# Kernel tuning notes

Measured on AMD Instinct MI355X. Metric: run time of the kernel, lower is better.

Reference implementation:

```python
import jax, jax.numpy as jnp
import numpy as np

N_AGENTS = 16      # args['num_agents']
BATCH = 8192       # args['n_rollout_threads'] -> number of independent graphs
OBS = 64           # cent_obs_shape[0] // n_nodes
HID = 128          # args['hidden_sizes'][0]
N_LAYERS = 2       # args['n_layers']
USE_RES = True     # args['use_res']


def _build_edges():
    # complete graph (no self loops) per graph, block-diagonal over BATCH graphs
    i, j = np.meshgrid(np.arange(N_AGENTS), np.arange(N_AGENTS), indexing='ij')
    m = i != j
    bs, bd = i[m], j[m]                      # [240]
    off = (np.arange(BATCH) * N_AGENTS)[:, None]
    src = (bs[None, :] + off).ravel().astype(np.int32)  # [BATCH*240]
    dst = (bd[None, :] + off).ravel().astype(np.int32)
    return src, dst


def setup_inputs() -> dict:
    key = jax.random.key(0)
    ks = jax.random.split(key, 5)
    N = BATCH * N_AGENTS
    src, dst = _build_edges()
    return {
        'cent_obs': jax.random.normal(ks[0], (N, OBS), jnp.float32),
        'w_emb': jax.random.normal(ks[1], (OBS, HID), jnp.float32) / np.sqrt(OBS).astype(np.float32),
        'b_emb': jnp.zeros((HID,), jnp.float32),
        'w_gcn': jax.random.normal(ks[2], (N_LAYERS, HID, HID), jnp.float32) / np.sqrt(HID).astype(np.float32),
        'b_gcn': jnp.zeros((N_LAYERS, HID), jnp.float32),
        'w_fc1': jax.random.normal(ks[3], (HID, 1), jnp.float32) / np.sqrt(HID).astype(np.float32),
        'b_fc1': jnp.zeros((1,), jnp.float32),
        'edge_src': jnp.asarray(src),
        'edge_dst': jnp.asarray(dst),
    }


def reference(cent_obs, w_emb, b_emb, w_gcn, b_gcn, w_fc1, b_fc1, edge_src, edge_dst):
    N = cent_obs.shape[0]
    # embedding_in
    x = cent_obs @ w_emb + b_emb                           # [N, HID]
    # GCNConv normalization with added self-loops (PyG default, sym norm)
    loop = jnp.arange(N, dtype=edge_src.dtype)
    src = jnp.concatenate([edge_src, loop])
    dst = jnp.concatenate([edge_dst, loop])
    deg = jax.ops.segment_sum(jnp.ones_like(dst, dtype=x.dtype), dst, num_segments=N)
    inv_sqrt = jax.lax.rsqrt(deg)
    norm = (inv_sqrt[src] * inv_sqrt[dst])[:, None]        # [E+N, 1]
    for l in range(N_LAYERS):
        h = x @ w_gcn[l]                                   # linear transform
        agg = jax.ops.segment_sum(h[src] * norm, dst, num_segments=N) + b_gcn[l]
        x = jnp.tanh(agg + x if USE_RES else agg)
    value = x @ w_fc1 + b_fc1                              # [N, 1]
    value = value.reshape(BATCH, -1)                       # [BATCH, n_nodes]
    return value.mean(axis=1).reshape(-1, 1)               # [BATCH, 1]
```

## Files before the change

kernel.cpp:

```cpp
#include <hip/hip_runtime.h>


#define N_GRAPHS 8192
#define BLOCK    512
#define GPB      16
#define NBLOCKS  (N_GRAPHS / GPB)

typedef __attribute__((ext_vector_type(8)))  short short8;
typedef __attribute__((ext_vector_type(4)))  float floatx4;
typedef __attribute__((ext_vector_type(16))) float floatx16;

#define MFMA16(a, b, c) __builtin_amdgcn_mfma_f32_16x16x32_bf16((a), (b), (c), 0, 0, 0)
#define MFMA32(a, b, c) __builtin_amdgcn_mfma_f32_32x32x16_bf16((a), (b), (c), 0, 0, 0)

#define EMB_LO   1024
#define GCN_BASE 2048
#define GCN_LO   2048

union fragu { unsigned int u[4]; short8 s8; };

__device__ __forceinline__ unsigned fbits(float x) {
  union { float f; unsigned u; } v; v.f = x; return v.u;
}
__device__ __forceinline__ float bitsf(unsigned u) {
  union { float f; unsigned u; } v; v.u = u; return v.f;
}
__device__ __forceinline__ void bsplit(float x, short& hi, short& lo) {
  unsigned hb = fbits(x) & 0xFFFF0000u;
  hi = (short)(hb >> 16);
  lo = (short)(fbits(x - bitsf(hb)) >> 16);
}
__device__ __forceinline__ unsigned hpack(unsigned b_odd, unsigned b_even) {
  return __builtin_amdgcn_perm(b_odd, b_even, 0x07060302u);
}
__device__ __forceinline__ void mk_frags(float4 a, float4 b, short8& hi, short8& lo) {
  fragu H, L;
  H.u[0] = hpack(fbits(a.y), fbits(a.x));
  H.u[1] = hpack(fbits(a.w), fbits(a.z));
  H.u[2] = hpack(fbits(b.y), fbits(b.x));
  H.u[3] = hpack(fbits(b.w), fbits(b.z));
  float l0 = a.x - bitsf(fbits(a.x) & 0xFFFF0000u);
  float l1 = a.y - bitsf(fbits(a.y) & 0xFFFF0000u);
  float l2 = a.z - bitsf(fbits(a.z) & 0xFFFF0000u);
  float l3 = a.w - bitsf(fbits(a.w) & 0xFFFF0000u);
  float l4 = b.x - bitsf(fbits(b.x) & 0xFFFF0000u);
  float l5 = b.y - bitsf(fbits(b.y) & 0xFFFF0000u);
  float l6 = b.z - bitsf(fbits(b.z) & 0xFFFF0000u);
  float l7 = b.w - bitsf(fbits(b.w) & 0xFFFF0000u);
  L.u[0] = hpack(fbits(l1), fbits(l0));
  L.u[1] = hpack(fbits(l3), fbits(l2));
  L.u[2] = hpack(fbits(l5), fbits(l4));
  L.u[3] = hpack(fbits(l7), fbits(l6));
  hi = H.s8; lo = L.s8;
}
__device__ __forceinline__ float fast_tanh(float z) {
  float e = __expf(2.0f * z);
  return 1.0f - __fdividef(2.0f, e + 1.0f);
}

__global__ __launch_bounds__(256) void gcn_prep(
    const float* __restrict__ w_emb, const float* __restrict__ w_gcn,
    unsigned short* __restrict__ wsS)
{
  int idx = blockIdx.x * 256 + threadIdx.x;
  if (idx >= 40960) return;
  int f = idx >> 3, j = idx & 7;
  const float* src;
  int hi_f, lo_f;
  if (f < 1024) {
    int ks = f >> 8, t = (f >> 6) & 3, L = f & 63;
    int k0 = ks * 16 + (L >> 5) * 8;
    int n  = t * 32 + (L & 31);
    src = w_emb + k0 * 128 + n;
    hi_f = f; lo_f = f + EMB_LO;
  } else {
    int f2 = f - 1024;
    int l = f2 >> 11, r = f2 & 2047;
    int kc = r >> 9, nt = (r >> 6) & 7, L = r & 63;
    int k0 = kc * 32 + (L >> 4) * 8;
    int n  = nt * 16 + (L & 15);
    src = w_gcn + l * 16384 + k0 * 128 + n;
    hi_f = GCN_BASE + l * 4096 + r; lo_f = hi_f + GCN_LO;
  }
  short h, l_;
  bsplit(src[j * 128], h, l_);
  wsS[hi_f * 8 + j] = (unsigned short)h;
  wsS[lo_f * 8 + j] = (unsigned short)l_;
}

__global__ __launch_bounds__(BLOCK, 4) void gcn_main(
    const float* __restrict__ obs,
    const float* __restrict__ b_emb,
    const float* __restrict__ b_gcn,
    const float* __restrict__ w_fc1,
    const float* __restrict__ b_fc1,
    const short8* __restrict__ tab,
    float* __restrict__ out)
{
  __shared__ short8 sEmb[2048];
  __shared__ short  sA[2 * 4 * 16 * 40];
  __shared__ float  sH[16][132];

  const int tid = threadIdx.x;
  const int w   = tid >> 6;
  const int L   = tid & 63;
  const int m32 = L & 31;
  const int kh  = L >> 5;
  const int c16 = L & 15;
  const int q   = L >> 4;
  const int gw  = blockIdx.x * GPB + 2 * w;

  const float* op = obs + (gw * 16 + m32) * 64 + kh * 8;
  float4 oa0 = *(const float4*)(op);
  float4 oa1 = *(const float4*)(op + 4);
  float4 ob0 = *(const float4*)(op + 16);
  float4 ob1 = *(const float4*)(op + 20);

  #pragma unroll
  for (int i = 0; i < 4; ++i) sEmb[i * BLOCK + tid] = tab[i * BLOCK + tid];

  floatx16 x[4];
  #pragma unroll
  for (int t = 0; t < 4; ++t) {
    float b = b_emb[t * 32 + m32];
    #pragma unroll
    for (int r = 0; r < 16; ++r) x[t][r] = b;
  }
  __syncthreads();

  #pragma unroll
  for (int s = 0; s < 4; ++s) {
    short8 ah, al;
    mk_frags(oa0, oa1, ah, al);
    oa0 = ob0; oa1 = ob1;
    if (s < 2) {
      ob0 = *(const float4*)(op + (s + 2) * 16);
      ob1 = *(const float4*)(op + (s + 2) * 16 + 4);
    }
    #pragma unroll
    for (int t = 0; t < 4; ++t) {
      int idx = (s * 4 + t) * 64 + L;
      short8 bh = sEmb[idx];
      short8 bl = sEmb[idx + EMB_LO];
      x[t] = MFMA32(ah, bh, x[t]);
      x[t] = MFMA32(al, bh, x[t]);
      x[t] = MFMA32(ah, bl, x[t]);
    }
  }

  #pragma unroll 1
  for (int l = 0; l < 2; ++l) {
    const short8* tbase = tab + GCN_BASE + l * 4096 + w * 64 + L;
    short8 bh[4], bl[4];
    #pragma unroll
    for (int kc = 0; kc < 4; ++kc) {
      bh[kc] = tbase[kc * 512];
      bl[kc] = tbase[kc * 512 + GCN_LO];
    }

    #pragma unroll
    for (int t = 0; t < 4; ++t) {
      float s0 = x[t][0], s1 = x[t][8];
      #pragma unroll
      for (int r = 1; r < 8; ++r) { s0 += x[t][r]; s1 += x[t][r + 8]; }
      s0 += __shfl_xor(s0, 32);
      s1 += __shfl_xor(s1, 32);
      s0 *= 0.0625f; s1 *= 0.0625f;
      #pragma unroll
      for (int rr = 0; rr < 2; ++rr) {
        float v = rr ? s1 : s0;
        unsigned hb = fbits(v) & 0xFFFF0000u;
        unsigned vb = (kh == 0) ? hb : fbits(v - bitsf(hb));
        unsigned nb = (unsigned)__shfl_xor((int)vb, 1);
        unsigned pw = hpack(nb, vb);
        if ((m32 & 1) == 0) {
          int si = kh * 2560 + t * 640 + (2 * w + rr) * 40 + m32;
          *(unsigned int*)&sA[si] = pw;
        }
      }
    }
    __syncthreads();

    floatx4 h = {0.f, 0.f, 0.f, 0.f};
    #pragma unroll
    for (int kc = 0; kc < 4; ++kc) {
      short8 ah = *(const short8*)&sA[kc * 640 + c16 * 40 + q * 8];
      short8 al = *(const short8*)&sA[2560 + kc * 640 + c16 * 40 + q * 8];
      h = MFMA16(ah, bh[kc], h);
      h = MFMA16(al, bh[kc], h);
      h = MFMA16(ah, bl[kc], h);
    }
    #pragma unroll
    for (int r = 0; r < 4; ++r)
      sH[q * 4 + r][w * 16 + c16] = h[r];
    __syncthreads();

    #pragma unroll
    for (int t = 0; t < 4; ++t) {
      float b  = b_gcn[l * 128 + t * 32 + m32];
      float zA = sH[2 * w][t * 32 + m32] + b;
      float zB = sH[2 * w + 1][t * 32 + m32] + b;
      #pragma unroll
      for (int r = 0; r < 8; ++r) {
        x[t][r]     = fast_tanh(x[t][r] + zA);
        x[t][r + 8] = fast_tanh(x[t][r + 8] + zB);
      }
    }
  }

  float vA = 0.f, vB = 0.f;
  #pragma unroll
  for (int t = 0; t < 4; ++t) {
    float wf = w_fc1[t * 32 + m32];
    float sA_ = 0.f, sB_ = 0.f;
    #pragma unroll
    for (int r = 0; r < 8; ++r) { sA_ += x[t][r]; sB_ += x[t][r + 8]; }
    vA = fmaf(sA_, wf, vA);
    vB = fmaf(sB_, wf, vB);
  }
  #pragma unroll
  for (int d = 32; d >= 1; d >>= 1) {
    vA += __shfl_xor(vA, d);
    vB += __shfl_xor(vB, d);
  }
  if (L == 0) {
    float bf = b_fc1[0];
    out[gw]     = vA * 0.0625f + bf;
    out[gw + 1] = vB * 0.0625f + bf;
  }
}

extern "C" void kernel_launch(void* const* d_in, const int* in_sizes, int n_in,
                              void* d_out, int out_size, void* d_ws, size_t ws_size,
                              hipStream_t stream) {
  const float* obs    = (const float*)d_in[0];
  const float* w_emb  = (const float*)d_in[1];
  const float* b_emb  = (const float*)d_in[2];
  const float* w_gcn  = (const float*)d_in[3];
  const float* b_gcn  = (const float*)d_in[4];
  const float* w_fc1  = (const float*)d_in[5];
  const float* b_fc1  = (const float*)d_in[6];
  float* out = (float*)d_out;

  gcn_prep<<<160, 256, 0, stream>>>(w_emb, w_gcn, (unsigned short*)d_ws);
  gcn_main<<<NBLOCKS, BLOCK, 0, stream>>>(obs, b_emb, b_gcn, w_fc1, b_fc1,
                                          (const short8*)d_ws, out);
}
```

Measured before the change: 120.3 us.

## Switch embedding to 16x16 MFMA with one graph per wave, raise occupancy

The embedding GEMM moves from 32x32x16 MFMA to 16x16x32 MFMA. Each wave now owns one graph instead of two, which shrinks per-thread accumulator state from four floatx16 to eight floatx4. The launch bounds raise the target to 6 blocks per CU, with twice as many blocks of half the graphs, and the GCN weight fragments are double-buffered instead of all preloaded. The goal is better latency hiding through higher occupancy and lower register pressure. The cost is extra shared-memory zero-padding and sync overhead per graph, and the prep kernel becomes thread-per-fragment.

```diff
diff --git a/kernel.cpp b/kernel.cpp
--- a/kernel.cpp
+++ b/kernel.cpp
@@ -3,15 +3,13 @@
 
 #define N_GRAPHS 8192
 #define BLOCK    512
-#define GPB      16
+#define GPB      8
 #define NBLOCKS  (N_GRAPHS / GPB)
 
-typedef __attribute__((ext_vector_type(8)))  short short8;
-typedef __attribute__((ext_vector_type(4)))  float floatx4;
-typedef __attribute__((ext_vector_type(16))) float floatx16;
+typedef __attribute__((ext_vector_type(8))) short short8;
+typedef __attribute__((ext_vector_type(4))) float floatx4;
 
 #define MFMA16(a, b, c) __builtin_amdgcn_mfma_f32_16x16x32_bf16((a), (b), (c), 0, 0, 0)
-#define MFMA32(a, b, c) __builtin_amdgcn_mfma_f32_32x32x16_bf16((a), (b), (c), 0, 0, 0)
 
 #define EMB_LO   1024
 #define GCN_BASE 2048
@@ -62,33 +60,33 @@
     const float* __restrict__ w_emb, const float* __restrict__ w_gcn,
     unsigned short* __restrict__ wsS)
 {
-  int idx = blockIdx.x * 256 + threadIdx.x;
-  if (idx >= 40960) return;
-  int f = idx >> 3, j = idx & 7;
+  int f = blockIdx.x * 256 + threadIdx.x;
+  if (f >= 5120) return;
   const float* src;
   int hi_f, lo_f;
   if (f < 1024) {
-    int ks = f >> 8, t = (f >> 6) & 3, L = f & 63;
-    int k0 = ks * 16 + (L >> 5) * 8;
-    int n  = t * 32 + (L & 31);
+    int kc = f >> 9, nt = (f >> 6) & 7, L = f & 63;
+    int k0 = kc * 32 + (L >> 4) * 8, n = nt * 16 + (L & 15);
     src = w_emb + k0 * 128 + n;
     hi_f = f; lo_f = f + EMB_LO;
   } else {
     int f2 = f - 1024;
     int l = f2 >> 11, r = f2 & 2047;
     int kc = r >> 9, nt = (r >> 6) & 7, L = r & 63;
-    int k0 = kc * 32 + (L >> 4) * 8;
-    int n  = nt * 16 + (L & 15);
+    int k0 = kc * 32 + (L >> 4) * 8, n = nt * 16 + (L & 15);
     src = w_gcn + l * 16384 + k0 * 128 + n;
     hi_f = GCN_BASE + l * 4096 + r; lo_f = hi_f + GCN_LO;
   }
-  short h, l_;
-  bsplit(src[j * 128], h, l_);
-  wsS[hi_f * 8 + j] = (unsigned short)h;
-  wsS[lo_f * 8 + j] = (unsigned short)l_;
-}
-
-__global__ __launch_bounds__(BLOCK, 4) void gcn_main(
+  #pragma unroll
+  for (int j = 0; j < 8; ++j) {
+    short h, l_;
+    bsplit(src[j * 128], h, l_);
+    wsS[hi_f * 8 + j] = (unsigned short)h;
+    wsS[lo_f * 8 + j] = (unsigned short)l_;
+  }
+}
+
+__global__ __launch_bounds__(BLOCK, 6) void gcn_main(
     const float* __restrict__ obs,
     const float* __restrict__ b_emb,
     const float* __restrict__ b_gcn,
@@ -99,135 +97,128 @@
 {
   __shared__ short8 sEmb[2048];
   __shared__ short  sA[2 * 4 * 16 * 40];
-  __shared__ float  sH[16][132];
+  __shared__ float  sH[8][132];
 
   const int tid = threadIdx.x;
   const int w   = tid >> 6;
   const int L   = tid & 63;
-  const int m32 = L & 31;
-  const int kh  = L >> 5;
   const int c16 = L & 15;
   const int q   = L >> 4;
-  const int gw  = blockIdx.x * GPB + 2 * w;
-
-  const float* op = obs + (gw * 16 + m32) * 64 + kh * 8;
-  float4 oa0 = *(const float4*)(op);
-  float4 oa1 = *(const float4*)(op + 4);
-  float4 ob0 = *(const float4*)(op + 16);
-  float4 ob1 = *(const float4*)(op + 20);
+  const int kh  = L >> 5;
+  const int group = blockIdx.x * GPB + w;
+
+  const float* op = obs + (group * 16 + c16) * 64 + q * 8;
+  float4 o00 = *(const float4*)(op);
+  float4 o01 = *(const float4*)(op + 4);
+  float4 o10 = *(const float4*)(op + 32);
+  float4 o11 = *(const float4*)(op + 36);
 
   #pragma unroll
   for (int i = 0; i < 4; ++i) sEmb[i * BLOCK + tid] = tab[i * BLOCK + tid];
-
-  floatx16 x[4];
-  #pragma unroll
-  for (int t = 0; t < 4; ++t) {
-    float b = b_emb[t * 32 + m32];
-    #pragma unroll
-    for (int r = 0; r < 16; ++r) x[t][r] = b;
+  {
+    unsigned int* za = (unsigned int*)sA;
+    #pragma unroll
+    for (int z = 0; z < 3; ++z) {
+      int i = z * BLOCK + tid;
+      if (i < 1280) {
+        int reg = i / 160, rm = i - reg * 160;
+        int r8 = rm / 20, cw = rm - r8 * 20;
+        za[reg * 320 + (r8 + 8) * 20 + cw] = 0;
+      }
+    }
+  }
+
+  floatx4 x[8];
+  #pragma unroll
+  for (int nt = 0; nt < 8; ++nt) {
+    float b = b_emb[nt * 16 + c16];
+    x[nt] = (floatx4){b, b, b, b};
   }
   __syncthreads();
 
   #pragma unroll
-  for (int s = 0; s < 4; ++s) {
+  for (int kc = 0; kc < 2; ++kc) {
     short8 ah, al;
-    mk_frags(oa0, oa1, ah, al);
-    oa0 = ob0; oa1 = ob1;
-    if (s < 2) {
-      ob0 = *(const float4*)(op + (s + 2) * 16);
-      ob1 = *(const float4*)(op + (s + 2) * 16 + 4);
-    }
-    #pragma unroll
-    for (int t = 0; t < 4; ++t) {
-      int idx = (s * 4 + t) * 64 + L;
+    mk_frags(kc ? o10 : o00, kc ? o11 : o01, ah, al);
+    #pragma unroll
+    for (int nt = 0; nt < 8; ++nt) {
+      int idx = kc * 512 + nt * 64 + L;
       short8 bh = sEmb[idx];
       short8 bl = sEmb[idx + EMB_LO];
-      x[t] = MFMA32(ah, bh, x[t]);
-      x[t] = MFMA32(al, bh, x[t]);
-      x[t] = MFMA32(ah, bl, x[t]);
+      x[nt] = MFMA16(ah, bh, x[nt]);
+      x[nt] = MFMA16(al, bh, x[nt]);
+      x[nt] = MFMA16(ah, bl, x[nt]);
     }
   }
 
   #pragma unroll 1
   for (int l = 0; l < 2; ++l) {
-    const short8* tbase = tab + GCN_BASE + l * 4096 + w * 64 + L;
-    short8 bh[4], bl[4];
+    const short8* tb = tab + GCN_BASE + l * 4096 + w * 64 + L;
+    short8 bhc[2], blc[2];
+    bhc[0] = tb[0];    blc[0] = tb[GCN_LO];
+    bhc[1] = tb[512];  blc[1] = tb[512 + GCN_LO];
+
+    #pragma unroll
+    for (int nt = 0; nt < 8; ++nt) {
+      float s = x[nt][0] + x[nt][1] + x[nt][2] + x[nt][3];
+      s += __shfl_xor(s, 16);
+      s += __shfl_xor(s, 32);
+      float v = s * 0.0625f;
+      unsigned hb = fbits(v) & 0xFFFF0000u;
+      unsigned vb = (kh == 0) ? hb : fbits(v - bitsf(hb));
+      unsigned nb = (unsigned)__shfl_xor((int)vb, 1);
+      if (((c16 & 1) | (q & 1)) == 0) {
+        unsigned pw = hpack(nb, vb);
+        int kc = nt >> 1, qp = ((nt & 1) << 1) | (c16 >> 3), j = c16 & 7;
+        int hw = kh * 2560 + kc * 640 + w * 40 + qp * 8 + j;
+        *(unsigned int*)&sA[hw] = pw;
+      }
+    }
+    __syncthreads();
+
+    floatx4 h0 = {0.f, 0.f, 0.f, 0.f};
+    floatx4 h1 = {0.f, 0.f, 0.f, 0.f};
     #pragma unroll
     for (int kc = 0; kc < 4; ++kc) {
-      bh[kc] = tbase[kc * 512];
-      bl[kc] = tbase[kc * 512 + GCN_LO];
-    }
-
-    #pragma unroll
-    for (int t = 0; t < 4; ++t) {
-      float s0 = x[t][0], s1 = x[t][8];
-      #pragma unroll
-      for (int r = 1; r < 8; ++r) { s0 += x[t][r]; s1 += x[t][r + 8]; }
-      s0 += __shfl_xor(s0, 32);
-      s1 += __shfl_xor(s1, 32);
-      s0 *= 0.0625f; s1 *= 0.0625f;
-      #pragma unroll
-      for (int rr = 0; rr < 2; ++rr) {
-        float v = rr ? s1 : s0;
-        unsigned hb = fbits(v) & 0xFFFF0000u;
-        unsigned vb = (kh == 0) ? hb : fbits(v - bitsf(hb));
-        unsigned nb = (unsigned)__shfl_xor((int)vb, 1);
-        unsigned pw = hpack(nb, vb);
-        if ((m32 & 1) == 0) {
-          int si = kh * 2560 + t * 640 + (2 * w + rr) * 40 + m32;
-          *(unsigned int*)&sA[si] = pw;
-        }
+      short8 bh = bhc[kc & 1], bl = blc[kc & 1];
+      if (kc < 2) {
+        bhc[kc & 1] = tb[(kc + 2) * 512];
+        blc[kc & 1] = tb[(kc + 2) * 512 + GCN_LO];
       }
-    }
-    __syncthreads();
-
-    floatx4 h = {0.f, 0.f, 0.f, 0.f};
-    #pragma unroll
-    for (int kc = 0; kc < 4; ++kc) {
       short8 ah = *(const short8*)&sA[kc * 640 + c16 * 40 + q * 8];
       short8 al = *(const short8*)&sA[2560 + kc * 640 + c16 * 40 + q * 8];
-      h = MFMA16(ah, bh[kc], h);
-      h = MFMA16(al, bh[kc], h);
-      h = MFMA16(ah, bl[kc], h);
-    }
-    #pragma unroll
-    for (int r = 0; r < 4; ++r)
-      sH[q * 4 + r][w * 16 + c16] = h[r];
+      floatx4& hh = (kc < 2) ? h0 : h1;
+      hh = MFMA16(ah, bh, hh);
+      hh = MFMA16(al, bh, hh);
+      hh = MFMA16(ah, bl, hh);
+    }
+    if (q < 2) {
+      float bgc = b_gcn[l * 128 + w * 16 + c16];
+      #pragma unroll
+      for (int r = 0; r < 4; ++r)
+        sH[q * 4 + r][w * 16 + c16] = h0[r] + h1[r] + bgc;
+    }
     __syncthreads();
 
     #pragma unroll
-    for (int t = 0; t < 4; ++t) {
-      float b  = b_gcn[l * 128 + t * 32 + m32];
-      float zA = sH[2 * w][t * 32 + m32] + b;
-      float zB = sH[2 * w + 1][t * 32 + m32] + b;
-      #pragma unroll
-      for (int r = 0; r < 8; ++r) {
-        x[t][r]     = fast_tanh(x[t][r] + zA);
-        x[t][r + 8] = fast_tanh(x[t][r + 8] + zB);
-      }
-    }
-  }
-
-  float vA = 0.f, vB = 0.f;
-  #pragma unroll
-  for (int t = 0; t < 4; ++t) {
-    float wf = w_fc1[t * 32 + m32];
-    float sA_ = 0.f, sB_ = 0.f;
-    #pragma unroll
-    for (int r = 0; r < 8; ++r) { sA_ += x[t][r]; sB_ += x[t][r + 8]; }
-    vA = fmaf(sA_, wf, vA);
-    vB = fmaf(sB_, wf, vB);
-  }
-  #pragma unroll
-  for (int d = 32; d >= 1; d >>= 1) {
-    vA += __shfl_xor(vA, d);
-    vB += __shfl_xor(vB, d);
-  }
-  if (L == 0) {
-    float bf = b_fc1[0];
-    out[gw]     = vA * 0.0625f + bf;
-    out[gw + 1] = vB * 0.0625f + bf;
-  }
+    for (int nt = 0; nt < 8; ++nt) {
+      float z = sH[w][nt * 16 + c16];
+      x[nt][0] = fast_tanh(x[nt][0] + z);
+      x[nt][1] = fast_tanh(x[nt][1] + z);
+      x[nt][2] = fast_tanh(x[nt][2] + z);
+      x[nt][3] = fast_tanh(x[nt][3] + z);
+    }
+  }
+
+  float v = 0.f;
+  #pragma unroll
+  for (int nt = 0; nt < 8; ++nt) {
+    float wf = w_fc1[nt * 16 + c16];
+    v = fmaf(x[nt][0] + x[nt][1] + x[nt][2] + x[nt][3], wf, v);
+  }
+  #pragma unroll
+  for (int d = 32; d >= 1; d >>= 1) v += __shfl_xor(v, d);
+  if (L == 0) out[group] = v * 0.0625f + b_fc1[0];
 }
 
 extern "C" void kernel_launch(void* const* d_in, const int* in_sizes, int n_in,
@@ -242,7 +233,7 @@
   const float* b_fc1  = (const float*)d_in[6];
   float* out = (float*)d_out;
 
-  gcn_prep<<<160, 256, 0, stream>>>(w_emb, w_gcn, (unsigned short*)d_ws);
+  gcn_prep<<<20, 256, 0, stream>>>(w_emb, w_gcn, (unsigned short*)d_ws);
   gcn_main<<<NBLOCKS, BLOCK, 0, stream>>>(obs, b_emb, b_gcn, w_fc1, b_fc1,
                                           (const short8*)d_ws, out);
 }
```

After: 122.9 us. 2.1% more time.
